# Optimization experiments

Measured on AMD Instinct MI355X. Metric: run time of the kernel, lower is better.

The kernel has to match this reference:

```python
import jax, jax.numpy as jnp
import numpy as np
from jax import lax
import math

B, C, L, H, K, NCONV = 64, 128, 400, 8, 7, 4  # batch, d_model, length, n_head, kernel, n_conv
DK = C // H
EPS = 1e-5


def setup_inputs() -> dict:
    key = jax.random.key(0)
    ks = jax.random.split(key, 16)
    inp = {
        'x': jax.random.normal(ks[0], (B, C, L), dtype=jnp.float32),
        'mask': jnp.ones((B, L), dtype=jnp.float32),
        'dw_w': jax.random.normal(ks[1], (NCONV, C, 1, K), dtype=jnp.float32) * 0.1,
        'dw_b': jnp.zeros((NCONV, C), dtype=jnp.float32),
        'pw_w': jax.random.normal(ks[2], (NCONV, C, C, 1), dtype=jnp.float32) * 0.05,
        'pw_b': jnp.zeros((NCONV, C), dtype=jnp.float32),
        'wq': jax.random.normal(ks[3], (C, C), dtype=jnp.float32) * 0.05,
        'bq': jnp.zeros((C,), dtype=jnp.float32),
        'wk': jax.random.normal(ks[4], (C, C), dtype=jnp.float32) * 0.05,
        'bk': jnp.zeros((C,), dtype=jnp.float32),
        'wv': jax.random.normal(ks[5], (C, C), dtype=jnp.float32) * 0.05,
        'bv': jnp.zeros((C,), dtype=jnp.float32),
        'wo': jax.random.normal(ks[6], (C, C), dtype=jnp.float32) * 0.05,
        'bo': jnp.zeros((C,), dtype=jnp.float32),
        'fc_w': jax.random.normal(ks[7], (C, C), dtype=jnp.float32) * 0.05,
        'fc_b': jnp.zeros((C,), dtype=jnp.float32),
        'ln_g': jnp.ones((C, L), dtype=jnpp.float32) if False else jnp.ones((C, L), dtype=jnp.float32),
        'ln_b': jnp.zeros((C, L), dtype=jnp.float32),
    }
    return inp


def _pos_encoding():
    i = jnp.arange(C, dtype=jnp.float32)
    even = (jnp.arange(C) % 2) == 0
    freqs = jnp.where(even, 10000.0 ** (-i / C), -(10000.0 ** ((1.0 - i) / C)))
    phases = jnp.where(even, 0.0, math.pi / 2.0)
    pos = jnp.arange(L, dtype=jnp.float32)
    return jnp.sin(pos[None, :] * freqs[:, None] + phases[:, None])  # (C, L)


def _layer_norm(o, g, b):
    # torch LayerNorm([d_model, length]): normalize each sample over (C, L) jointly
    mu = jnp.mean(o, axis=(1, 2), keepdims=True)
    var = jnp.mean((o - mu) ** 2, axis=(1, 2), keepdims=True)
    return (o - mu) * lax.rsqrt(var + EPS) * g[None] + b[None]


def _dwsep_conv(o, dw, db, pw, pb):
    # depthwise: groups=C, kernel (C,1,K), 'same' padding
    y = lax.conv_general_dilated(o, dw, window_strides=(1,), padding=[(K // 2, K // 2)],
                                 dimension_numbers=('NCH', 'OIH', 'NCH'), feature_group_count=C)
    y = y + db[None, :, None]
    # pointwise 1x1 conv
    y = jnp.einsum('oc,bcl->bol', pw[:, :, 0], y) + pb[None, :, None]
    return y


def _attention(o, mask, wq, bq, wk, bk, wv, bv, wo, bo):
    xt = jnp.transpose(o, (0, 2, 1))  # (B, L, C)
    q = (xt @ wq.T + bq).reshape(B, L, H, DK)
    k = (xt @ wk.T + bk).reshape(B, L, H, DK)
    v = (xt @ wv.T + bv).reshape(B, L, H, DK)
    atten = jnp.einsum('blhd,bmhd->bhlm', q, k) / math.sqrt(C)  # note: sqrt(d_model), faithful
    m = mask[:, None, None, :]  # (B,1,1,L)
    atten = atten * m + (1.0 - m) * -1e30
    atten = jax.nn.softmax(atten, axis=-1)
    out = jnp.einsum('bhlm,bmhd->blhd', atten, v).reshape(B, L, C)
    out = out @ wo.T + bo
    return jnp.transpose(out, (0, 2, 1))  # (B, C, L)


def reference(x, mask, dw_w, dw_b, pw_w, pw_b, wq, bq, wk, bk, wv, bv, wo, bo, fc_w, fc_b, ln_g, ln_b):
    out = x + _pos_encoding()[None]
    res = out
    out = _layer_norm(out, ln_g, ln_b)
    for i in range(NCONV):
        out = _dwsep_conv(out, dw_w[i], dw_b[i], pw_w[i], pw_b[i])
        out = jax.nn.relu(out)
        out = res + out
        res = out
        out = _layer_norm(out, ln_g, ln_b)
    out = _attention(out, mask, wq, bq, wk, bk, wv, bv, wo, bo)
    out = res + out
    res = out
    out = _layer_norm(out, ln_g, ln_b)
    out = jnp.einsum('bcl,ec->bel', out, fc_w) + fc_b[None, :, None]
    out = jax.nn.relu(out)
    out = res + out
    return out
```

## Files before the change

### kernel.cpp

```cpp
#include <hip/hip_runtime.h>
#include <math.h>

constexpr int BN = 64;
constexpr int CC = 128;
constexpr int LL = 400;
constexpr int DK = 16;
constexpr int KK = 7;
constexpr int CL = CC * LL;
constexpr int NBCL = BN * CL;
constexpr float EPSV = 1e-5f;
constexpr float INV_N = 1.0f / (float)CL;
constexpr float BIGL = 1.4427e30f;

typedef __attribute__((ext_vector_type(8))) short bf16x8;
typedef __attribute__((ext_vector_type(4))) float f32x4;

__device__ __forceinline__ short f2bf(float f) {
  unsigned u = __builtin_bit_cast(unsigned, f);
  u = (u + 0x7fffu + ((u >> 16) & 1u)) >> 16;
  return (short)u;
}
__device__ __forceinline__ float bf2f(unsigned short u) {
  return __builtin_bit_cast(float, (unsigned)u << 16);
}
__device__ __forceinline__ unsigned pkbf(float hi, float lo) {
  return __builtin_amdgcn_perm(__builtin_bit_cast(unsigned, hi),
                               __builtin_bit_cast(unsigned, lo), 0x07060302u);
}

__global__ __launch_bounds__(256) void prep_kernel(
    const float* __restrict__ pw_w, const float* __restrict__ wq,
    const float* __restrict__ wk, const float* __restrict__ wv,
    const float* __restrict__ wo, const float* __restrict__ fcw,
    const float* __restrict__ pw_b, const float* __restrict__ dw_b,
    const float* __restrict__ mask,
    unsigned short* __restrict__ wf, float* __restrict__ pose,
    float* __restrict__ stats, float* __restrict__ beff,
    float* __restrict__ maddb)
{
  int blk = blockIdx.x;
  if (blk < 576) {
    int idx = blk * 256 + threadIdx.x;
    int mat = idx >> 14;
    int e = idx & 16383;
    const float* src;
    if (mat < 4)       src = pw_w + mat * 16384;
    else if (mat == 4) src = wq;
    else if (mat == 5) src = wk;
    else if (mat == 6) src = wv;
    else if (mat == 7) src = wo;
    else               src = fcw;
    int o = e >> 7, c = e & 127;
    int t = (o >> 4) * 4 + (c >> 5);
    int quad = (c >> 3) & 3, col = o & 15, j = c & 7;
    wf[mat * 16384 + t * 512 + (quad * 16 + col) * 8 + j] = (unsigned short)f2bf(src[e]);
  } else if (blk < 776) {
    int idx = (blk - 576) * 256 + threadIdx.x;
    int c = idx / LL, l = idx - c * LL;
    float fc = (float)c;
    float freq, ph;
    if ((c & 1) == 0) { freq = powf(10000.f, -fc / (float)CC);        ph = 0.f; }
    else              { freq = -powf(10000.f, (1.f - fc) / (float)CC); ph = 1.5707963267948966f; }
    pose[idx] = sinf((float)l * freq + ph);
  } else if (blk == 776) {
    for (int i = threadIdx.x; i < 1024; i += 256) stats[i] = 0.f;
  } else if (blk == 777) {
    for (int t = threadIdx.x; t < 512; t += 256) {
      int i = t >> 7, o = t & 127;
      float a = pw_b[t];
      const float* wrow = pw_w + (size_t)i * 16384 + o * 128;
      const float* db = dw_b + i * 128;
      for (int c2 = 0; c2 < 128; c2++) a += wrow[c2] * db[c2];
      beff[t] = a;
    }
  } else {
    int idx = (blk - 778) * 256 + threadIdx.x;
    int b = idx / 416, m = idx - b * 416;
    maddb[idx] = (m < LL) ? (mask[b * LL + m] - 1.f) * BIGL : -BIGL;
  }
}

__global__ __launch_bounds__(256) void addpos_stats_kernel(
    const float* __restrict__ x, const float* __restrict__ pose,
    unsigned short* __restrict__ res, float* __restrict__ stats)
{
  int idx4 = blockIdx.x * 256 + threadIdx.x;
  int b = idx4 / (CL / 4);
  int cl4 = (idx4 - b * (CL / 4)) * 4;
  const float4 xv = *reinterpret_cast<const float4*>(&x[(size_t)idx4 * 4]);
  const float4 pv = *reinterpret_cast<const float4*>(&pose[cl4]);
  ushort4 h;
  h.x = (unsigned short)f2bf(xv.x + pv.x);
  h.y = (unsigned short)f2bf(xv.y + pv.y);
  h.z = (unsigned short)f2bf(xv.z + pv.z);
  h.w = (unsigned short)f2bf(xv.w + pv.w);
  *reinterpret_cast<ushort4*>(&res[(size_t)idx4 * 4]) = h;
  float v0 = bf2f(h.x), v1 = bf2f(h.y), v2 = bf2f(h.z), v3 = bf2f(h.w);
  float s1 = v0 + v1 + v2 + v3;
  float s2 = v0 * v0 + v1 * v1 + v2 * v2 + v3 * v3;
  #pragma unroll
  for (int off = 32; off > 0; off >>= 1) {
    s1 += __shfl_down(s1, off);
    s2 += __shfl_down(s2, off);
  }
  __shared__ float r1[4], r2[4];
  int wv = threadIdx.x >> 6, lane = threadIdx.x & 63;
  if (lane == 0) { r1[wv] = s1; r2[wv] = s2; }
  __syncthreads();
  if (threadIdx.x == 0) {
    atomicAdd(&stats[b * 2 + 0], r1[0] + r1[1] + r1[2] + r1[3]);
    atomicAdd(&stats[b * 2 + 1], r2[0] + r2[1] + r2[2] + r2[3]);
  }
}

template<int XMODE>
__device__ __forceinline__ void stage_x(
    short* __restrict__ XsF, const unsigned short* __restrict__ Xb,
    int j0, const float* __restrict__ lng, const float* __restrict__ lnb,
    const float* __restrict__ dww, float mu, float rstd, int tid)
{
  for (int idx = tid; idx < 1024; idx += 512) {
    int c = idx >> 3;
    int l8 = (idx & 7) * 8;
    int col0 = j0 + l8;
    short hv[8];
    if (XMODE == 2) {
      const unsigned short* rp = Xb + c * LL;
      const float* gp = lng + c * LL;
      const float* bp = lnb + c * LL;
      float xn[16];
      #pragma unroll
      for (int g4 = 0; g4 < 4; g4++) {
        int p0 = col0 - 4 + g4 * 4;
        int pc = p0 < 0 ? 0 : (p0 > LL - 4 ? LL - 4 : p0);
        const ushort4 rv = *reinterpret_cast<const ushort4*>(&rp[pc]);
        const float4 gv = *reinterpret_cast<const float4*>(&gp[pc]);
        const float4 bv4 = *reinterpret_cast<const float4*>(&bp[pc]);
        float rr[4] = {bf2f(rv.x), bf2f(rv.y), bf2f(rv.z), bf2f(rv.w)};
        float gg[4] = {gv.x, gv.y, gv.z, gv.w};
        float bbv[4] = {bv4.x, bv4.y, bv4.z, bv4.w};
        #pragma unroll
        for (int e = 0; e < 4; e++) {
          int p = p0 + e;
          float v = (rr[e] - mu) * rstd * gg[e] + bbv[e];
          xn[g4 * 4 + e] = (p >= 0 && p < LL) ? v : 0.f;
        }
      }
      float w7[KK];
      #pragma unroll
      for (int j = 0; j < KK; j++) w7[j] = dww[c * KK + j];
      #pragma unroll
      for (int e = 0; e < 8; e++) {
        float a = 0.f;
        #pragma unroll
        for (int jj = 0; jj < KK; jj++) a += w7[jj] * xn[e + jj + 1];
        hv[e] = f2bf(a);
      }
    } else {
      bool valid = col0 < LL;
      int col0c = valid ? col0 : 0;
      const unsigned short* xp = Xb + c * LL + col0c;
      const ushort4 u0 = *reinterpret_cast<const ushort4*>(&xp[0]);
      const ushort4 u1 = *reinterpret_cast<const ushort4*>(&xp[4]);
      unsigned short uu[8] = {u0.x, u0.y, u0.z, u0.w, u1.x, u1.y, u1.z, u1.w};
      if (XMODE == 1) {
        #pragma unroll
        for (int e = 0; e < 8; e++) hv[e] = valid ? (short)uu[e] : (short)0;
      } else {
        const float* gp = lng + c * LL + col0c;
        const float* bp = lnb + c * LL + col0c;
        const float4 g0 = *reinterpret_cast<const float4*>(&gp[0]);
        const float4 g1 = *reinterpret_cast<const float4*>(&gp[4]);
        const float4 b0 = *reinterpret_cast<const float4*>(&bp[0]);
        const float4 b1 = *reinterpret_cast<const float4*>(&bp[4]);
        float gg[8] = {g0.x, g0.y, g0.z, g0.w, g1.x, g1.y, g1.z, g1.w};
        float bbv[8] = {b0.x, b0.y, b0.z, b0.w, b1.x, b1.y, b1.z, b1.w};
        #pragma unroll
        for (int e = 0; e < 8; e++) {
          float v = (bf2f(uu[e]) - mu) * rstd * gg[e] + bbv[e];
          hv[e] = valid ? f2bf(v) : (short)0;
        }
      }
    }
    int t = (l8 >> 4) * 4 + (c >> 5);
    int quad = (c >> 3) & 3;
    int j = c & 7;
    int base = t * 512 + quad * 128 + j;
    int colb = l8 & 15;
    #pragma unroll
    for (int e = 0; e < 8; e++) XsF[base + (colb + e) * 8] = hv[e];
  }
}

template<int XMODE, int OMODE, bool RELU, bool ADDRES, bool STATS>
__device__ __forceinline__ void gemm_body(
    const unsigned short* __restrict__ Wf, const unsigned short* __restrict__ Xv,
    const float* __restrict__ bias, const unsigned short* __restrict__ resid,
    const float* __restrict__ lng, const float* __restrict__ lnb,
    const float* __restrict__ dww,
    const float* __restrict__ statsIn, float* __restrict__ statsOut,
    void* __restrict__ Yv)
{
  __shared__ short XsF[16 * 512];
  __shared__ float red[16];
  int tid = threadIdx.x;
  int bb = blockIdx.y;
  int j0 = blockIdx.x * 64;
  int w = tid >> 6, lane = tid & 63;
  bf16x8 af[4];
  #pragma unroll
  for (int kt = 0; kt < 4; kt++)
    af[kt] = *reinterpret_cast<const bf16x8*>(&Wf[(w * 4 + kt) * 512 + lane * 8]);
  float mu = 0.f, rstd = 0.f;
  if (XMODE != 1) {
    float s1 = statsIn[bb * 2 + 0], s2 = statsIn[bb * 2 + 1];
    mu = s1 * INV_N;
    rstd = rsqrtf(s2 * INV_N - mu * mu + EPSV);
  }
  stage_x<XMODE>(XsF, Xv + (size_t)bb * CL, j0, lng, lnb, dww, mu, rstd, tid);
  __syncthreads();
  int col = lane & 15, quad = lane >> 4;
  f32x4 acc[4];
  #pragma unroll
  for (int lf = 0; lf < 4; lf++) acc[lf] = (f32x4){0.f, 0.f, 0.f, 0.f};
  #pragma unroll
  for (int kt = 0; kt < 4; kt++) {
    #pragma unroll
    for (int lf = 0; lf < 4; lf++) {
      bf16x8 bx = *reinterpret_cast<const bf16x8*>(&XsF[(lf * 4 + kt) * 512 + lane * 8]);
      acc[lf] = __builtin_amdgcn_mfma_f32_16x16x32_bf16(af[kt], bx, acc[lf], 0, 0, 0);
    }
  }
  int obase = w * 16;
  float bv[4];
  #pragma unroll
  for (int r = 0; r < 4; r++) bv[r] = bias[obase + quad * 4 + r];
  float lsum = 0.f, lsq = 0.f;
  #pragma unroll
  for (int lf = 0; lf < 4; lf++) {
    if (j0 + lf * 16 < LL) {
      int l = j0 + lf * 16 + col;
      if (OMODE == 2) {
        short4 hv4 = {f2bf(acc[lf][0] + bv[0]), f2bf(acc[lf][1] + bv[1]),
                      f2bf(acc[lf][2] + bv[2]), f2bf(acc[lf][3] + bv[3])};
        *reinterpret_cast<short4*>(
            &((unsigned short*)Yv)[(((size_t)bb * 8 + w) * LL + l) * 16 + quad * 4]) = hv4;
      } else {
        #pragma unroll
        for (int r = 0; r < 4; r++) {
          float v = acc[lf][r] + bv[r];
          if (RELU) v = fmaxf(v, 0.f);
          size_t oidx = (size_t)bb * CL + (size_t)(obase + quad * 4 + r) * LL + l;
          if (ADDRES) v += bf2f(resid[oidx]);
          if (OMODE == 1) {
            unsigned short hb = (unsigned short)f2bf(v);
            ((unsigned short*)Yv)[oidx] = hb;
            if (STATS) { float vf = bf2f(hb); lsum += vf; lsq += vf * vf; }
          } else {
            ((float*)Yv)[oidx] = v;
            if (STATS) { lsum += v; lsq += v * v; }
          }
        }
      }
    }
  }
  if (STATS) {
    #pragma unroll
    for (int off = 32; off > 0; off >>= 1) {
      lsum += __shfl_down(lsum, off);
      lsq  += __shfl_down(lsq, off);
    }
    if (lane == 0) { red[w * 2] = lsum; red[w * 2 + 1] = lsq; }
    __syncthreads();
    if (tid == 0) {
      float a = 0.f, b2 = 0.f;
      #pragma unroll
      for (int w2 = 0; w2 < 8; w2++) { a += red[w2 * 2]; b2 += red[w2 * 2 + 1]; }
      atomicAdd(&statsOut[bb * 2 + 0], a);
      atomicAdd(&statsOut[bb * 2 + 1], b2);
    }
  }
}

template<int XMODE, int OMODE, bool RELU, bool ADDRES, bool STATS>
__global__ __launch_bounds__(512) void gemmM(
    const unsigned short* __restrict__ Wf, const unsigned short* __restrict__ X,
    const float* __restrict__ bias, const unsigned short* __restrict__ resid,
    const float* __restrict__ lng, const float* __restrict__ lnb,
    const float* __restrict__ dww,
    const float* __restrict__ statsIn, float* __restrict__ statsOut,
    void* __restrict__ Y)
{
  gemm_body<XMODE, OMODE, RELU, ADDRES, STATS>(
      Wf, X, bias, resid, lng, lnb, dww, statsIn, statsOut, Y);
}

__global__ __launch_bounds__(512) void qkv_kernel(
    const unsigned short* __restrict__ wf,
    const float* __restrict__ bq, const float* __restrict__ bk, const float* __restrict__ bv,
    const unsigned short* __restrict__ X,
    const float* __restrict__ lng, const float* __restrict__ lnb,
    const float* __restrict__ statsIn,
    unsigned short* __restrict__ qt, unsigned short* __restrict__ kt,
    unsigned short* __restrict__ vb)
{
  if (blockIdx.z == 0)
    gemm_body<0, 2, false, false, false>(wf + 4 * 16384, X, bq, nullptr, lng, lnb,
                                         nullptr, statsIn, nullptr, qt);
  else if (blockIdx.z == 1)
    gemm_body<0, 2, false, false, false>(wf + 5 * 16384, X, bk, nullptr, lng, lnb,
                                         nullptr, statsIn, nullptr, kt);
  else
    gemm_body<0, 1, false, false, false>(wf + 6 * 16384, X, bv, nullptr, lng, lnb,
                                         nullptr, statsIn, nullptr, vb);
}

__global__ __launch_bounds__(256) void attn_kernel(
    const unsigned short* __restrict__ qt, const unsigned short* __restrict__ kt,
    const unsigned short* __restrict__ vb, const float* __restrict__ maddb,
    unsigned short* __restrict__ ao)
{
  __shared__ short Pl[4][2][64 * 40];
  int bh = blockIdx.x;
  int b = bh >> 3, h = bh & 7;
  int wave = threadIdx.x >> 6, lane = threadIdx.x & 63;
  int tile = blockIdx.y * 4 + wave;
  if (tile >= 7) return;
  int col = lane & 15;
  int quad = lane >> 4;
  int l0 = tile * 64;
  size_t trow = ((size_t)b * 8 + h) * LL;
  size_t base = ((size_t)b * CC + h * DK) * LL;
  const unsigned short* qp = qt + trow * 16;
  const unsigned short* kp = kt + trow * 16;
  const unsigned short* vp = vb + base;
  const float* mb = maddb + (size_t)b * 416;

  bf16x8 qf[4];
  #pragma unroll
  for (int f = 0; f < 4; f++) {
    bf16x8 v = {};
    if (quad < 2) {
      int l = l0 + f * 16 + col; int lc = l < LL ? l : LL - 1;
      v = *reinterpret_cast<const bf16x8*>(&qp[lc * 16 + quad * 8]);
    }
    qf[f] = v;
  }
  f32x4 of[4];
  float psum[4];
  #pragma unroll
  for (int f = 0; f < 4; f++) {
    of[f] = (f32x4){0.f, 0.f, 0.f, 0.f};
    psum[f] = 0.f;
  }
  const float scale2 = 0.08838834764831845f * 1.4426950408889634f;

  int buf = 0;
  for (int m0 = 0; m0 < LL; m0 += 32, buf ^= 1) {
    bf16x8 kf0 = {}, kf1 = {};
    if (quad < 2) {
      int mc0 = m0 + col < LL ? m0 + col : LL - 1;
      int mc1 = m0 + 16 + col < LL ? m0 + 16 + col : LL - 1;
      kf0 = *reinterpret_cast<const bf16x8*>(&kp[mc0 * 16 + quad * 8]);
      kf1 = *reinterpret_cast<const bf16x8*>(&kp[mc1 * 16 + quad * 8]);
    }
    bf16x8 vf;
    {
      int ms = m0 + quad * 8; if (ms > LL - 8) ms = LL - 8;
      vf = *reinterpret_cast<const bf16x8*>(&vp[col * LL + ms]);
    }
    const float4 a4 = *reinterpret_cast<const float4*>(&mb[m0 + quad * 4]);
    const float4 b4 = *reinterpret_cast<const float4*>(&mb[m0 + 16 + quad * 4]);
    float madd[8] = {a4.x, a4.y, a4.z, a4.w, b4.x, b4.y, b4.z, b4.w};
    #pragma unroll
    for (int f = 0; f < 4; f++) {
      f32x4 z = {0.f, 0.f, 0.f, 0.f};
      f32x4 s0 = __builtin_amdgcn_mfma_f32_16x16x32_bf16(kf0, qf[f], z, 0, 0, 0);
      f32x4 s1 = __builtin_amdgcn_mfma_f32_16x16x32_bf16(kf1, qf[f], z, 0, 0, 0);
      float p[8];
      #pragma unroll
      for (int r = 0; r < 4; r++) {
        p[r]     = exp2f(s0[r] * scale2 + madd[r]);
        p[4 + r] = exp2f(s1[r] * scale2 + madd[4 + r]);
      }
      float ps = 0.f;
      #pragma unroll
      for (int i = 0; i < 8; i++) ps += p[i];
      psum[f] += ps;
      short* row = &Pl[wave][buf][(f * 16 + col) * 40];
      short4 h0 = __builtin_bit_cast(short4, make_uint2(pkbf(p[1], p[0]), pkbf(p[3], p[2])));
      short4 h1 = __builtin_bit_cast(short4, make_uint2(pkbf(p[5], p[4]), pkbf(p[7], p[6])));
      *reinterpret_cast<short4*>(&row[quad * 4])      = h0;
      *reinterpret_cast<short4*>(&row[16 + quad * 4]) = h1;
    }
    #pragma unroll
    for (int f = 0; f < 4; f++) {
      bf16x8 pf = *reinterpret_cast<const bf16x8*>(&Pl[wave][buf][(f * 16 + col) * 40 + quad * 8]);
      of[f] = __builtin_amdgcn_mfma_f32_16x16x32_bf16(vf, pf, of[f], 0, 0, 0);
    }
  }
  #pragma unroll
  for (int f = 0; f < 4; f++) {
    float s = psum[f];
    s += __shfl_xor(s, 16);
    s += __shfl_xor(s, 32);
    float inv = 1.f / s;
    int lf = l0 + f * 16;
    if (lf < LL) {
      #pragma unroll
      for (int r = 0; r < 4; r++)
        ao[base + (size_t)(quad * 4 + r) * LL + lf + col] =
            (unsigned short)f2bf(of[f][r] * inv);
    }
  }
}

extern "C" void kernel_launch(void* const* d_in, const int* in_sizes, int n_in,
                              void* d_out, int out_size, void* d_ws, size_t ws_size,
                              hipStream_t stream) {
  const float* x    = (const float*)d_in[0];
  const float* mask = (const float*)d_in[1];
  const float* dw_w = (const float*)d_in[2];
  const float* dw_b = (const float*)d_in[3];
  const float* pw_w = (const float*)d_in[4];
  const float* pw_b = (const float*)d_in[5];
  const float* wq   = (const float*)d_in[6];
  const float* bq   = (const float*)d_in[7];
  const float* wk   = (const float*)d_in[8];
  const float* bk   = (const float*)d_in[9];
  const float* wvp  = (const float*)d_in[10];
  const float* bv   = (const float*)d_in[11];
  const float* wo   = (const float*)d_in[12];
  const float* bo   = (const float*)d_in[13];
  const float* fcw  = (const float*)d_in[14];
  const float* fcb  = (const float*)d_in[15];
  const float* lng  = (const float*)d_in[16];
  const float* lnb  = (const float*)d_in[17];
  float* out = (float*)d_out;
  float* ws  = (float*)d_ws;

  float* stats = ws;
  float* pose  = ws + 1024;
  float* beff  = pose + 51200;
  float* maddb = beff + 512;
  unsigned short* wf = (unsigned short*)(maddb + 64 * 416);
  unsigned short* r0 = wf + 9 * 16384;
  unsigned short* r1 = r0 + NBCL;
  unsigned short* qt = r1 + NBCL;
  unsigned short* kt = qt + NBCL;
  unsigned short* vbf = kt + NBCL;
  unsigned short* tb = vbf + NBCL;

  prep_kernel<<<882, 256, 0, stream>>>(pw_w, wq, wk, wvp, wo, fcw, pw_b, dw_b,
                                       mask, wf, pose, stats, beff, maddb);
  addpos_stats_kernel<<<3200, 256, 0, stream>>>(x, pose, r0, stats);

  unsigned short* rin = r0;
  unsigned short* rout = r1;
  for (int i = 0; i < 4; i++) {
    gemmM<2, 1, true, true, true><<<dim3(7, BN), 512, 0, stream>>>(
        wf + i * 16384, rin, beff + i * CC, rin, lng, lnb,
        dw_w + i * CC * KK, stats + i * 128, stats + (i + 1) * 128, rout);
    unsigned short* t = rin; rin = rout; rout = t;
  }
  qkv_kernel<<<dim3(7, BN, 3), 512, 0, stream>>>(
      wf, bq, bk, bv, rin, lng, lnb, stats + 4 * 128, qt, kt, vbf);
  attn_kernel<<<dim3(512, 2), 256, 0, stream>>>(qt, kt, vbf, maddb, tb);
  gemmM<1, 1, false, true, true><<<dim3(7, BN), 512, 0, stream>>>(
      wf + 7 * 16384, tb, bo, rin, nullptr, nullptr, nullptr,
      nullptr, stats + 5 * 128, rout);
  gemmM<0, 0, true, true, false><<<dim3(7, BN), 512, 0, stream>>>(
      wf + 8 * 16384, rout, fcb, rout, lng, lnb, nullptr,
      stats + 5 * 128, nullptr, out);
}
```

Before: 262.2 us.

## Split attention key range across wave pairs and merge partial sums in LDS

Each 64-query tile of the attention kernel is now processed by two waves, each covering half of the key range. The second wave hands its partial outputs and row sums to the first through shared memory, and the grid doubles in y so that more waves run in parallel. The kernel also switches to the hardware exp2 builtin, shrinks the P scratch buffer so each 16-row fragment is stored and consumed immediately, and adds an occupancy hint to launch bounds. In exchange it adds a block-wide barrier, an LDS reduction step, and some wasted work on padded key blocks past L.

```diff
diff --git a/kernel.cpp b/kernel.cpp
--- a/kernel.cpp
+++ b/kernel.cpp
@@ -14,6 +14,15 @@
 
 typedef __attribute__((ext_vector_type(8))) short bf16x8;
 typedef __attribute__((ext_vector_type(4))) float f32x4;
+
+#if defined(__has_builtin)
+#if __has_builtin(__builtin_amdgcn_exp2f)
+#define EXP2F(x) __builtin_amdgcn_exp2f(x)
+#endif
+#endif
+#ifndef EXP2F
+#define EXP2F(x) exp2f(x)
+#endif
 
 __device__ __forceinline__ short f2bf(float f) {
   unsigned u = __builtin_bit_cast(unsigned, f);
@@ -315,20 +324,22 @@
                                          nullptr, statsIn, nullptr, vb);
 }
 
-__global__ __launch_bounds__(256) void attn_kernel(
+__global__ __launch_bounds__(256, 8) void attn_kernel(
     const unsigned short* __restrict__ qt, const unsigned short* __restrict__ kt,
     const unsigned short* __restrict__ vb, const float* __restrict__ maddb,
     unsigned short* __restrict__ ao)
 {
-  __shared__ short Pl[4][2][64 * 40];
+  __shared__ short Pl[4][2][640];
+  __shared__ float Mg[2][64][20];
   int bh = blockIdx.x;
   int b = bh >> 3, h = bh & 7;
-  int wave = threadIdx.x >> 6, lane = threadIdx.x & 63;
-  int tile = blockIdx.y * 4 + wave;
-  if (tile >= 7) return;
-  int col = lane & 15;
-  int quad = lane >> 4;
-  int l0 = tile * 64;
+  int w = threadIdx.x >> 6, lane = threadIdx.x & 63;
+  int pair = w >> 1, half = w & 1;
+  int tile = blockIdx.y * 2 + pair;
+  bool live = tile < 7;
+  int tile_c = live ? tile : 6;
+  int col = lane & 15, quad = lane >> 4;
+  int l0 = tile_c * 64;
   size_t trow = ((size_t)b * 8 + h) * LL;
   size_t base = ((size_t)b * CC + h * DK) * LL;
   const unsigned short* qp = qt + trow * 16;
@@ -355,8 +366,9 @@
   }
   const float scale2 = 0.08838834764831845f * 1.4426950408889634f;
 
-  int buf = 0;
-  for (int m0 = 0; m0 < LL; m0 += 32, buf ^= 1) {
+  int mstart = half ? 224 : 0;
+  int mend   = half ? 416 : 224;
+  for (int m0 = mstart; m0 < mend; m0 += 32) {
     bf16x8 kf0 = {}, kf1 = {};
     if (quad < 2) {
       int mc0 = m0 + col < LL ? m0 + col : LL - 1;
@@ -380,37 +392,53 @@
       float p[8];
       #pragma unroll
       for (int r = 0; r < 4; r++) {
-        p[r]     = exp2f(s0[r] * scale2 + madd[r]);
-        p[4 + r] = exp2f(s1[r] * scale2 + madd[4 + r]);
+        p[r]     = EXP2F(s0[r] * scale2 + madd[r]);
+        p[4 + r] = EXP2F(s1[r] * scale2 + madd[4 + r]);
       }
       float ps = 0.f;
       #pragma unroll
       for (int i = 0; i < 8; i++) ps += p[i];
       psum[f] += ps;
-      short* row = &Pl[wave][buf][(f * 16 + col) * 40];
+      short* row = &Pl[w][f & 1][col * 40];
       short4 h0 = __builtin_bit_cast(short4, make_uint2(pkbf(p[1], p[0]), pkbf(p[3], p[2])));
       short4 h1 = __builtin_bit_cast(short4, make_uint2(pkbf(p[5], p[4]), pkbf(p[7], p[6])));
       *reinterpret_cast<short4*>(&row[quad * 4])      = h0;
       *reinterpret_cast<short4*>(&row[16 + quad * 4]) = h1;
-    }
+      bf16x8 pf = *reinterpret_cast<const bf16x8*>(&Pl[w][f & 1][col * 40 + quad * 8]);
+      of[f] = __builtin_amdgcn_mfma_f32_16x16x32_bf16(vf, pf, of[f], 0, 0, 0);
+    }
+  }
+  if (half == 1) {
+    float* mg = &Mg[pair][lane][0];
     #pragma unroll
     for (int f = 0; f < 4; f++) {
-      bf16x8 pf = *reinterpret_cast<const bf16x8*>(&Pl[wave][buf][(f * 16 + col) * 40 + quad * 8]);
-      of[f] = __builtin_amdgcn_mfma_f32_16x16x32_bf16(vf, pf, of[f], 0, 0, 0);
-    }
-  }
-  #pragma unroll
-  for (int f = 0; f < 4; f++) {
-    float s = psum[f];
-    s += __shfl_xor(s, 16);
-    s += __shfl_xor(s, 32);
-    float inv = 1.f / s;
-    int lf = l0 + f * 16;
-    if (lf < LL) {
-      #pragma unroll
-      for (int r = 0; r < 4; r++)
-        ao[base + (size_t)(quad * 4 + r) * LL + lf + col] =
-            (unsigned short)f2bf(of[f][r] * inv);
+      #pragma unroll
+      for (int r = 0; r < 4; r++) mg[f * 4 + r] = of[f][r];
+      mg[16 + f] = psum[f];
+    }
+  }
+  __syncthreads();
+  if (half == 0 && live) {
+    const float* mg = &Mg[pair][lane][0];
+    #pragma unroll
+    for (int f = 0; f < 4; f++) {
+      #pragma unroll
+      for (int r = 0; r < 4; r++) of[f][r] += mg[f * 4 + r];
+      psum[f] += mg[16 + f];
+    }
+    #pragma unroll
+    for (int f = 0; f < 4; f++) {
+      float s = psum[f];
+      s += __shfl_xor(s, 16);
+      s += __shfl_xor(s, 32);
+      float inv = 1.f / s;
+      int lf = l0 + f * 16;
+      if (lf < LL) {
+        #pragma unroll
+        for (int r = 0; r < 4; r++)
+          ao[base + (size_t)(quad * 4 + r) * LL + lf + col] =
+              (unsigned short)f2bf(of[f][r] * inv);
+      }
     }
   }
 }
@@ -465,7 +493,7 @@
   }
   qkv_kernel<<<dim3(7, BN, 3), 512, 0, stream>>>(
       wf, bq, bk, bv, rin, lng, lnb, stats + 4 * 128, qt, kt, vbf);
-  attn_kernel<<<dim3(512, 2), 256, 0, stream>>>(qt, kt, vbf, maddb, tb);
+  attn_kernel<<<dim3(512, 4), 256, 0, stream>>>(qt, kt, vbf, maddb, tb);
   gemmM<1, 1, false, true, true><<<dim3(7, BN), 512, 0, stream>>>(
       wf + 7 * 16384, tb, bo, rin, nullptr, nullptr, nullptr,
       nullptr, stats + 5 * 128, rout);
```

Result: slower. 317.7 us (+21.1%).
